# Optimization experiments

Measured on AMD Instinct MI355X. Metric: run time of the kernel, lower is better.

The kernel has to match this reference:

```python
import jax, jax.numpy as jnp
import numpy as np

N_BLOCK = 3; EMBED = 256; N_HEAD = 8; HEAD = EMBED // N_HEAD
N_AGENT = 8; SEQ = 256; BATCH = 64; ACT_DIM = 32
DECAY_SCALE = 1.0
EPS = 1e-6


def _decay_matrix():
    # Per-head decay kappas as in Mava Sable, decay over timesteps (pos // n_agent), causal mask.
    gammas = (1.0 - jnp.exp(jnp.linspace(jnp.log(1.0 / 32.0), jnp.log(1.0 / 512.0), N_HEAD))) * DECAY_SCALE
    t = (jnp.arange(SEQ) // N_AGENT).astype(jnp.float32)
    diff = t[:, None] - t[None, :]
    causal = jnp.arange(SEQ)[:, None] >= jnp.arange(SEQ)[None, :]
    return jnp.where(causal[None], gammas[:, None, None] ** diff[None], 0.0)  # [H,S,S]


def rmsnorm(x, scale):
    return x * jax.lax.rsqrt(jnp.mean(x * x, -1, keepdims=True) + EPS) * scale


def groupnorm(x, scale, bias):
    # GroupNorm with n_head groups over the feature dim, per position.
    B, S, E = x.shape
    xg = x.reshape(B, S, N_HEAD, HEAD)
    mu = xg.mean(-1, keepdims=True)
    var = ((xg - mu) ** 2).mean(-1, keepdims=True)
    xn = ((xg - mu) * jax.lax.rsqrt(var + 1e-5)).reshape(B, S, E)
    return xn * scale + bias


def retention(q_in, k_in, v_in, wq, wk, wv, wg, wo, gns, gnb, decay):
    # Parallel multi-scale retention: (Q K^T * D) V, groupnorm, swish gate from query input.
    B, S, E = q_in.shape
    q = (q_in @ wq).reshape(B, S, N_HEAD, HEAD).transpose(0, 2, 1, 3)
    k = (k_in @ wk).reshape(B, S, N_HEAD, HEAD).transpose(0, 2, 1, 3) / jnp.sqrt(jnp.float32(HEAD))
    v = (v_in @ wv).reshape(B, S, N_HEAD, HEAD).transpose(0, 2, 1, 3)
    scores = jnp.einsum('bhnd,bhmd->bhnm', q, k) * decay[None]
    ret = jnp.einsum('bhnm,bhmd->bhnd', scores, v)
    ret = groupnorm(ret.transpose(0, 2, 1, 3).reshape(B, S, E), gns, gnb)
    return (jax.nn.swish(q_in @ wg) * ret) @ wo


def swiglu(x, wg, w1, w2):
    return (jax.nn.swish(x @ wg) * (x @ w1)) @ w2


def forward(action, obs_rep, w_enc, ln0, wq1, wk1, wv1, wg1, wo1, gns1, gnb1, ln1,
            wq2, wk2, wv2, wg2, wo2, gns2, gnb2, ln2, swg, sw1, sw2, ln3,
            hw1, hb1, hln, hw2, hb2):
    decay = _decay_matrix()
    x = rmsnorm(jax.nn.gelu(action @ w_enc), ln0)
    for b in range(N_BLOCK):
        r1 = retention(x, x, x, wq1[b], wk1[b], wv1[b], wg1[b], wo1[b], gns1[b], gnb1[b], decay)
        x = rmsnorm(x + r1, ln1[b])
        r2 = retention(obs_rep, x, x, wq2[b], wk2[b], wv2[b], wg2[b], wo2[b], gns2[b], gnb2[b], decay)
        x = rmsnorm(obs_rep + r2, ln2[b])
        x = rmsnorm(x + swiglu(x, swg[b], sw1[b], sw2[b]), ln3[b])
    h = rmsnorm(jax.nn.gelu(x @ hw1 + hb1), hln)
    return h @ hw2 + hb2


def setup_inputs() -> dict:
    key = jax.random.key(0)
    ks = jax.random.split(key, 24)
    E, A, NB = EMBED, ACT_DIM, N_BLOCK
    s = 0.02
    return {
        'action': jax.random.uniform(ks[0], (BATCH, SEQ, A), jnp.float32),
        'obs_rep': jax.random.normal(ks[1], (BATCH, SEQ, E), jnp.float32),
        'w_enc': jax.random.normal(ks[2], (A, E), jnp.float32) * s,
        'ln0': jnp.ones((E,), jnp.float32),
        'wq1': jax.random.normal(ks[3], (NB, E, E), jnp.float32) * s,
        'wk1': jax.random.normal(ks[4], (NB, E, E), jnp.float32) * s,
        'wv1': jax.random.normal(ks[5], (NB, E, E), jnp.float32) * s,
        'wg1': jax.random.normal(ks[6], (NB, E, E), jnp.float32) * s,
        'wo1': jax.random.normal(ks[7], (NB, E, E), jnp.float32) * s,
        'gns1': jnp.ones((NB, E), jnp.float32),
        'gnb1': jnp.zeros((NB, E), jnp.float32),
        'ln1': jnp.ones((NB, E), jnp.float32),
        'wq2': jax.random.normal(ks[8], (NB, E, E), jnp.float32) * s,
        'wk2': jax.random.normal(ks[9], (NB, E, E), jnp.float32) * s,
        'wv2': jax.random.normal(ks[10], (NB, E, E), jnp.float32) * s,
        'wg2': jax.random.normal(ks[11], (NB, E, E), jnp.float32) * s,
        'wo2': jax.random.normal(ks[12], (NB, E, E), jnp.float32) * s,
        'gns2': jnp.ones((NB, E), jnp.float32),
        'gnb2': jnp.zeros((NB, E), jnp.float32),
        'ln2': jnp.ones((NB, E), jnp.float32),
        'swg': jax.random.normal(ks[13], (NB, E, E), jnp.float32) * s,
        'sw1': jax.random.normal(ks[14], (NB, E, E), jnp.float32) * s,
        'sw2': jax.random.normal(ks[15], (NB, E, E), jnp.float32) * s,
        'ln3': jnp.ones((NB, E), jnp.float32),
        'hw1': jax.random.normal(ks[16], (E, E), jnp.float32) * s,
        'hb1': jnp.zeros((E,), jnp.float32),
        'hln': jnp.ones((E,), jnp.float32),
        'hw2': jax.random.normal(ks[17], (E, A), jnp.float32) * s,
        'hb2': jnp.zeros((A,), jnp.float32),
    }


def reference(action, obs_rep, w_enc, ln0, wq1, wk1, wv1, wg1, wo1, gns1, gnb1, ln1,
              wq2, wk2, wv2, wg2, wo2, gns2, gnb2, ln2, swg, sw1, sw2, ln3,
              hw1, hb1, hln, hw2, hb2):
    return forward(action, obs_rep, w_enc, ln0, wq1, wk1, wv1, wg1, wo1, gns1, gnb1, ln1,
                   wq2, wk2, wv2, wg2, wo2, gns2, gnb2, ln2, swg, sw1, sw2, ln3,
                   hw1, hb1, hln, hw2, hb2)
```

## Files before the change

kernel.cpp:

```cpp
#include <hip/hip_runtime.h>
#include <cstdint>
#include <cmath>

typedef __attribute__((ext_vector_type(8))) short short8;
typedef __attribute__((ext_vector_type(4))) float floatx4;

#define DEV static __device__ __forceinline__

DEV float bf2f(uint16_t u) {
    union { uint32_t i; float f; } v; v.i = ((uint32_t)u) << 16; return v.f;
}
DEV uint16_t f2bf(float f) {
    union { float f; uint32_t i; } v; v.f = f;
    uint32_t r = (v.i + 0x7FFFu + ((v.i >> 16) & 1u)) >> 16;
    return (uint16_t)r;
}
DEV float swishf(float x) { return x / (1.f + __expf(-x)); }
DEV float geluf(float x) {
    const float c = 0.7978845608028654f;
    float t = tanhf(c * (x + 0.044715f * x * x * x));
    return 0.5f * x * (1.f + t);
}

#define CHUNK_E 8192
#define MAT_E   65536
#define APAD    264


struct TArg { const float* src[15]; };

__global__ __launch_bounds__(256) void tpose_k(TArg ta, uint16_t* __restrict__ arena) {
    int z = blockIdx.z;
    const float* src; uint16_t* dst;
    if (z == 0) {
        if (blockIdx.y) return;
        src = ta.src[0]; dst = arena;
    } else if (z <= 39) {
        int q = z - 1; int ti = q / 3, s = q % 3;
        src = ta.src[1 + ti] + (size_t)s * 65536;
        dst = arena + CHUNK_E + (size_t)(ti * 3 + s) * MAT_E;
    } else {
        src = ta.src[14]; dst = arena + CHUNK_E + (size_t)39 * MAT_E;
    }
    int k0 = blockIdx.y << 5;
    int n0 = blockIdx.x << 6;
    __shared__ __align__(16) uint16_t tile[32][72];
    int t = threadIdx.x;
    {
        int r = t >> 3, c = (t & 7) << 3;
        const float* s0 = src + (size_t)(k0 + r) * 256 + n0 + c;
        float4 f0 = *(const float4*)s0;
        float4 f1 = *(const float4*)(s0 + 4);
        tile[r][c + 0] = f2bf(f0.x); tile[r][c + 1] = f2bf(f0.y);
        tile[r][c + 2] = f2bf(f0.z); tile[r][c + 3] = f2bf(f0.w);
        tile[r][c + 4] = f2bf(f1.x); tile[r][c + 5] = f2bf(f1.y);
        tile[r][c + 6] = f2bf(f1.z); tile[r][c + 7] = f2bf(f1.w);
    }
    __syncthreads();
    {
        int n = t >> 2, c = (t & 3) << 3;
        uint16_t tmp[8];
#pragma unroll
        for (int j = 0; j < 8; ++j) tmp[j] = tile[c + j][n];
        *(uint4*)&dst[(size_t)(k0 >> 5) * CHUNK_E + (size_t)(n0 + n) * 32 + c] = *(uint4*)tmp;
    }
}

struct SegArgs {
    const float* action; const float* obs;
    uint16_t *actb, *obsb, *xb, *bq, *bk, *bv, *bg, *brg;
    const float *ln0, *hb1, *hln, *hw2, *hb2;
    float* outp;
    float l2g[8];
};

enum { EP_NONE = 0, EP_GELU_RMS = 1, EP_RESID_RMS = 2 };
enum { EP2_NONE = 0, EP2_SWIGLU = 1 };

template<int EPI, int K, int LDA, bool OG, int LDO, bool RL>
DEV void gemm_u(int m0,
                const uint16_t* __restrict__ A,
                const uint16_t* __restrict__ Wt,
                uint16_t* __restrict__ Og,
                uint16_t* __restrict__ Ol,
                const float* __restrict__ bias,
                const uint16_t* __restrict__ Rg,
                const uint16_t* __restrict__ Rl,
                const float* __restrict__ lnw,
                float (&rowsum)[8][32])
{
    const int t = threadIdx.x;
    const int w = t >> 6, lane = t & 63, l16 = lane & 15, lg = lane >> 4;
    constexpr int NC = K / 32;

    floatx4 acc[2][2];
#pragma unroll
    for (int i = 0; i < 2; ++i)
#pragma unroll
        for (int j = 0; j < 2; ++j) acc[i][j] = (floatx4){0.f, 0.f, 0.f, 0.f};

#pragma unroll
    for (int kc = 0; kc < NC; ++kc) {
        short8 aF[2], bF[2];
#pragma unroll
        for (int rt = 0; rt < 2; ++rt) {
            int row = (rt << 4) + l16;
            if constexpr (LDA != 0)
                aF[rt] = *(const short8*)(A + (size_t)row * LDA + (kc << 5) + (lg << 3));
            else
                aF[rt] = *(const short8*)(A + (size_t)(m0 + row) * K + (kc << 5) + (lg << 3));
        }
#pragma unroll
        for (int ct = 0; ct < 2; ++ct)
            bF[ct] = *(const short8*)(Wt + (size_t)kc * CHUNK_E +
                                      (size_t)((w << 5) + (ct << 4) + l16) * 32 + (lg << 3));
#pragma unroll
        for (int rt = 0; rt < 2; ++rt)
#pragma unroll
            for (int ct = 0; ct < 2; ++ct)
                acc[rt][ct] = __builtin_amdgcn_mfma_f32_16x16x32_bf16(
                    aF[rt], bF[ct], acc[rt][ct], 0, 0, 0);
    }

    float v[2][2][4];
#pragma unroll
    for (int rt = 0; rt < 2; ++rt)
#pragma unroll
        for (int ct = 0; ct < 2; ++ct)
#pragma unroll
            for (int r = 0; r < 4; ++r) {
                int row = (rt << 4) + (lg << 2) + r;
                int col = (w << 5) + (ct << 4) + l16;
                float x = acc[rt][ct][r];
                if constexpr (EPI == EP_GELU_RMS) {
                    if (bias) x += bias[col];
                    x = geluf(x);
                }
                if constexpr (EPI == EP_RESID_RMS) {
                    if constexpr (RL) x += bf2f(Rl[(size_t)row * APAD + col]);
                    else              x += bf2f(Rg[(size_t)(m0 + row) * 256 + col]);
                }
                v[rt][ct][r] = x;
            }

    if constexpr (EPI == EP_GELU_RMS || EPI == EP_RESID_RMS) {
#pragma unroll
        for (int rt = 0; rt < 2; ++rt)
#pragma unroll
            for (int r = 0; r < 4; ++r) {
                float p = v[rt][0][r] * v[rt][0][r] + v[rt][1][r] * v[rt][1][r];
                p += __shfl_xor(p, 1, 64); p += __shfl_xor(p, 2, 64);
                p += __shfl_xor(p, 4, 64); p += __shfl_xor(p, 8, 64);
                int row = (rt << 4) + (lg << 2) + r;
                if (l16 == 0) rowsum[w][row] = p;
            }
        __syncthreads();
#pragma unroll
        for (int rt = 0; rt < 2; ++rt)
#pragma unroll
            for (int r = 0; r < 4; ++r) {
                int row = (rt << 4) + (lg << 2) + r;
                float tot = rowsum[0][row] + rowsum[1][row] + rowsum[2][row] + rowsum[3][row]
                          + rowsum[4][row] + rowsum[5][row] + rowsum[6][row] + rowsum[7][row];
                float rn = rsqrtf(tot * (1.f / 256.f) + 1e-6f);
#pragma unroll
                for (int ct = 0; ct < 2; ++ct) {
                    int col = (w << 5) + (ct << 4) + l16;
                    uint16_t bb = f2bf(v[rt][ct][r] * rn * lnw[col]);
                    if constexpr (OG)
                        Og[(size_t)(m0 + row) * 256 + col] = bb;
                    if constexpr (LDO != 0)
                        Ol[(size_t)row * LDO + col] = bb;
                }
            }
        __syncthreads();
    } else {
#pragma unroll
        for (int rt = 0; rt < 2; ++rt)
#pragma unroll
            for (int ct = 0; ct < 2; ++ct)
#pragma unroll
                for (int r = 0; r < 4; ++r) {
                    int row = (rt << 4) + (lg << 2) + r;
                    int col = (w << 5) + (ct << 4) + l16;
                    uint16_t bb = f2bf(v[rt][ct][r]);
                    if constexpr (OG)
                        Og[(size_t)(m0 + row) * 256 + col] = bb;
                    if constexpr (LDO != 0)
                        Ol[(size_t)row * LDO + col] = bb;
                }
    }
}

template<int EPI, int LDA>
DEV void gemm2_u(int m0, const uint16_t* __restrict__ A,
                 const uint16_t* __restrict__ W1, const uint16_t* __restrict__ W2,
                 uint16_t* __restrict__ O1, uint16_t* __restrict__ O2,
                 uint16_t* __restrict__ Ol)
{
    const int t = threadIdx.x;
    const int w = t >> 6, lane = t & 63, l16 = lane & 15, lg = lane >> 4;

    floatx4 a1[2][2], a2[2][2];
#pragma unroll
    for (int i = 0; i < 2; ++i)
#pragma unroll
        for (int j = 0; j < 2; ++j) {
            a1[i][j] = (floatx4){0.f, 0.f, 0.f, 0.f};
            a2[i][j] = (floatx4){0.f, 0.f, 0.f, 0.f};
        }

#pragma unroll
    for (int kc = 0; kc < 8; ++kc) {
        short8 aF[2], b1[2], b2[2];
#pragma unroll
        for (int rt = 0; rt < 2; ++rt) {
            int row = (rt << 4) + l16;
            if constexpr (LDA != 0)
                aF[rt] = *(const short8*)(A + (size_t)row * LDA + (kc << 5) + (lg << 3));
            else
                aF[rt] = *(const short8*)(A + (size_t)(m0 + row) * 256 + (kc << 5) + (lg << 3));
        }
        size_t woff = (size_t)kc * CHUNK_E + (size_t)((w << 5) + l16) * 32 + (lg << 3);
#pragma unroll
        for (int ct = 0; ct < 2; ++ct) {
            b1[ct] = *(const short8*)(W1 + woff + (size_t)(ct << 4) * 32);
            b2[ct] = *(const short8*)(W2 + woff + (size_t)(ct << 4) * 32);
        }
#pragma unroll
        for (int rt = 0; rt < 2; ++rt)
#pragma unroll
            for (int ct = 0; ct < 2; ++ct) {
                a1[rt][ct] = __builtin_amdgcn_mfma_f32_16x16x32_bf16(aF[rt], b1[ct], a1[rt][ct], 0, 0, 0);
                a2[rt][ct] = __builtin_amdgcn_mfma_f32_16x16x32_bf16(aF[rt], b2[ct], a2[rt][ct], 0, 0, 0);
            }
    }

#pragma unroll
    for (int rt = 0; rt < 2; ++rt)
#pragma unroll
        for (int ct = 0; ct < 2; ++ct)
#pragma unroll
            for (int r = 0; r < 4; ++r) {
                int row = (rt << 4) + (lg << 2) + r;
                int col = (w << 5) + (ct << 4) + l16;
                if constexpr (EPI == EP2_NONE) {
                    size_t idx = (size_t)(m0 + row) * 256 + col;
                    O1[idx] = f2bf(a1[rt][ct][r]);
                    O2[idx] = f2bf(a2[rt][ct][r]);
                } else {
                    Ol[(size_t)row * APAD + col] = f2bf(swishf(a1[rt][ct][r]) * a2[rt][ct][r]);
                }
            }
}

template<int LDA>
DEV void gemm4_u(int m0, const uint16_t* __restrict__ A,
                 const uint16_t* __restrict__ W0, const uint16_t* __restrict__ W1,
                 const uint16_t* __restrict__ W2, const uint16_t* __restrict__ W3,
                 uint16_t* __restrict__ O0, uint16_t* __restrict__ O1,
                 uint16_t* __restrict__ O2, uint16_t* __restrict__ O3)
{
    const int t = threadIdx.x;
    const int w = t >> 6, lane = t & 63, l16 = lane & 15, lg = lane >> 4;
    const uint16_t* Wm[4] = {W0, W1, W2, W3};
    uint16_t* Om[4] = {O0, O1, O2, O3};

    floatx4 acc[4][2][2];
#pragma unroll
    for (int m = 0; m < 4; ++m)
#pragma unroll
        for (int i = 0; i < 2; ++i)
#pragma unroll
            for (int j = 0; j < 2; ++j) acc[m][i][j] = (floatx4){0.f, 0.f, 0.f, 0.f};

#pragma unroll
    for (int kc = 0; kc < 8; ++kc) {
        short8 aF[2];
#pragma unroll
        for (int rt = 0; rt < 2; ++rt) {
            int row = (rt << 4) + l16;
            if constexpr (LDA != 0)
                aF[rt] = *(const short8*)(A + (size_t)row * LDA + (kc << 5) + (lg << 3));
            else
                aF[rt] = *(const short8*)(A + (size_t)(m0 + row) * 256 + (kc << 5) + (lg << 3));
        }
        size_t woff = (size_t)kc * CHUNK_E + (size_t)((w << 5) + l16) * 32 + (lg << 3);
        short8 bF[4][2];
#pragma unroll
        for (int m = 0; m < 4; ++m)
#pragma unroll
            for (int ct = 0; ct < 2; ++ct)
                bF[m][ct] = *(const short8*)(Wm[m] + woff + (size_t)(ct << 4) * 32);
#pragma unroll
        for (int m = 0; m < 4; ++m)
#pragma unroll
            for (int rt = 0; rt < 2; ++rt)
#pragma unroll
                for (int ct = 0; ct < 2; ++ct)
                    acc[m][rt][ct] = __builtin_amdgcn_mfma_f32_16x16x32_bf16(
                        aF[rt], bF[m][ct], acc[m][rt][ct], 0, 0, 0);
    }

#pragma unroll
    for (int m = 0; m < 4; ++m)
#pragma unroll
        for (int rt = 0; rt < 2; ++rt)
#pragma unroll
            for (int ct = 0; ct < 2; ++ct)
#pragma unroll
                for (int r = 0; r < 4; ++r) {
                    int row = (rt << 4) + (lg << 2) + r;
                    int col = (w << 5) + (ct << 4) + l16;
                    Om[m][(size_t)(m0 + row) * 256 + col] = f2bf(acc[m][rt][ct][r]);
                }
}

template<int LDA1>
DEV void gemm22_u(int m0, const uint16_t* __restrict__ A1, const uint16_t* __restrict__ A2,
                  const uint16_t* __restrict__ W0, const uint16_t* __restrict__ W1,
                  const uint16_t* __restrict__ W2, const uint16_t* __restrict__ W3,
                  uint16_t* __restrict__ O0, uint16_t* __restrict__ O1,
                  uint16_t* __restrict__ O2, uint16_t* __restrict__ O3)
{
    const int t = threadIdx.x;
    const int w = t >> 6, lane = t & 63, l16 = lane & 15, lg = lane >> 4;
    const uint16_t* Wm[4] = {W0, W1, W2, W3};
    uint16_t* Om[4] = {O0, O1, O2, O3};

    floatx4 acc[4][2][2];
#pragma unroll
    for (int m = 0; m < 4; ++m)
#pragma unroll
        for (int i = 0; i < 2; ++i)
#pragma unroll
            for (int j = 0; j < 2; ++j) acc[m][i][j] = (floatx4){0.f, 0.f, 0.f, 0.f};

#pragma unroll
    for (int kc = 0; kc < 8; ++kc) {
        short8 a1F[2], a2F[2];
#pragma unroll
        for (int rt = 0; rt < 2; ++rt) {
            int row = (rt << 4) + l16;
            a1F[rt] = *(const short8*)(A1 + (size_t)row * LDA1 + (kc << 5) + (lg << 3));
            a2F[rt] = *(const short8*)(A2 + (size_t)(m0 + row) * 256 + (kc << 5) + (lg << 3));
        }
        size_t woff = (size_t)kc * CHUNK_E + (size_t)((w << 5) + l16) * 32 + (lg << 3);
        short8 bF[4][2];
#pragma unroll
        for (int m = 0; m < 4; ++m)
#pragma unroll
            for (int ct = 0; ct < 2; ++ct)
                bF[m][ct] = *(const short8*)(Wm[m] + woff + (size_t)(ct << 4) * 32);
#pragma unroll
        for (int m = 0; m < 4; ++m)
#pragma unroll
            for (int rt = 0; rt < 2; ++rt)
#pragma unroll
                for (int ct = 0; ct < 2; ++ct)
                    acc[m][rt][ct] = __builtin_amdgcn_mfma_f32_16x16x32_bf16(
                        (m < 2) ? a1F[rt] : a2F[rt], bF[m][ct], acc[m][rt][ct], 0, 0, 0);
    }

#pragma unroll
    for (int m = 0; m < 4; ++m)
#pragma unroll
        for (int rt = 0; rt < 2; ++rt)
#pragma unroll
            for (int ct = 0; ct < 2; ++ct)
#pragma unroll
                for (int r = 0; r < 4; ++r) {
                    int row = (rt << 4) + (lg << 2) + r;
                    int col = (w << 5) + (ct << 4) + l16;
                    Om[m][(size_t)(m0 + row) * 256 + col] = f2bf(acc[m][rt][ct][r]);
                }
}

DEV int rowbase(int blk) { return (blk & 63) * 256 + (blk >> 6) * 32; }


__global__ __launch_bounds__(512, 4) void seg0_k(SegArgs sa, const uint16_t* __restrict__ wenc,
                                                 const uint16_t* __restrict__ wq,
                                                 const uint16_t* __restrict__ wk,
                                                 const uint16_t* __restrict__ wv,
                                                 const uint16_t* __restrict__ wg)
{
    __shared__ float rowsum[8][32];
    __shared__ __align__(16) uint16_t actS[32][40];
    __shared__ __align__(16) uint16_t T0[32][APAD];
    const int t = threadIdx.x;
    const int m0 = rowbase(blockIdx.x);
    if (t < 256) {
        int r = t >> 3, c = (t & 7) << 2;
        float4 f = *(const float4*)(sa.action + (size_t)(m0 + r) * 32 + c);
        uint16_t tmp[4] = { f2bf(f.x), f2bf(f.y), f2bf(f.z), f2bf(f.w) };
        *(uint2*)&actS[r][c] = *(uint2*)tmp;
    }
    {
        const float4* ob = (const float4*)sa.obs + (size_t)m0 * 64;
        uint2* od = (uint2*)sa.obsb + (size_t)m0 * 64;
#pragma unroll
        for (int j = 0; j < 4; ++j) {
            float4 f = ob[(j << 9) + t];
            uint16_t tmp[4] = { f2bf(f.x), f2bf(f.y), f2bf(f.z), f2bf(f.w) };
            od[(j << 9) + t] = *(uint2*)tmp;
        }
    }
    __syncthreads();
    gemm_u<EP_GELU_RMS, 32, 40, true, APAD, false>(m0, &actS[0][0], wenc,
        sa.xb, &T0[0][0], nullptr, nullptr, nullptr, sa.ln0, rowsum);
    gemm4_u<APAD>(m0, &T0[0][0], wq, wk, wv, wg, sa.bq, sa.bk, sa.bv, sa.bg);
}

__global__ __launch_bounds__(512, 4) void attn_k(SegArgs sa, const float* __restrict__ gns,
                                                 const float* __restrict__ gnb)
{
    __shared__ __align__(16) uint16_t QS[256][40];
    __shared__ __align__(16) uint16_t Ks[256][40];
    __shared__ __align__(16) uint16_t Vt[32][264];
    const int b = blockIdx.x & 63, h = blockIdx.x >> 6;
    const float l2g = sa.l2g[h];
    const int t = threadIdx.x, w = t >> 6, lane = t & 63, l16 = lane & 15, lg = lane >> 4;
    const size_t base = ((size_t)b * 256) * 256 + (size_t)h * 32;
    const uint16_t *q = sa.bq, *kbuf = sa.bk, *vbuf = sa.bv, *g = sa.bg;
    uint16_t* out = sa.brg;

    if (t < 256) {
        const uint4* qr = (const uint4*)(q + base + (size_t)t * 256);
        *(uint4*)&QS[t][0] = qr[0]; *(uint4*)&QS[t][8] = qr[1];
        *(uint4*)&QS[t][16] = qr[2]; *(uint4*)&QS[t][24] = qr[3];
        const uint4* kr = (const uint4*)(kbuf + base + (size_t)t * 256);
        *(uint4*)&Ks[t][0] = kr[0]; *(uint4*)&Ks[t][8] = kr[1];
        *(uint4*)&Ks[t][16] = kr[2]; *(uint4*)&Ks[t][24] = kr[3];
    } else {
        int c = t - 256;
        union { uint4 v4[4]; uint16_t u[32]; } vv;
        const uint4* vr = (const uint4*)(vbuf + base + (size_t)c * 256);
        vv.v4[0] = vr[0]; vv.v4[1] = vr[1]; vv.v4[2] = vr[2]; vv.v4[3] = vr[3];
#pragma unroll
        for (int d = 0; d < 32; ++d) Vt[d][c] = vv.u[d];
    }
    __syncthreads();

    const int iA = w, iB = 15 - w;
    short8 qFA = *(const short8*)&QS[(iA << 4) + l16][lg << 3];
    short8 qFB = *(const short8*)&QS[(iB << 4) + l16][lg << 3];

    const float invsq = 0.17677669529663687f;

    floatx4 raccA[2], raccB[2];
    raccA[0] = (floatx4){0,0,0,0}; raccA[1] = (floatx4){0,0,0,0};
    raccB[0] = (floatx4){0,0,0,0}; raccB[1] = (floatx4){0,0,0,0};

    auto do_strip = [&](int si, short8 qF, floatx4 (&racc)[2]) {
        const int jtmax = ((si << 4) + 15) >> 5;
        for (int jt = 0; jt <= jtmax; ++jt) {
            const int j0 = jt << 5;
            floatx4 sacc[2];
            sacc[0] = (floatx4){0,0,0,0}; sacc[1] = (floatx4){0,0,0,0};
            short8 kF[2];
#pragma unroll
            for (int ct = 0; ct < 2; ++ct)
                kF[ct] = *(const short8*)&Ks[j0 + (ct << 4) + l16][lg << 3];
#pragma unroll
            for (int ct = 0; ct < 2; ++ct)
                sacc[ct] = __builtin_amdgcn_mfma_f32_16x16x32_bf16(
                    qF, kF[ct], sacc[ct], 0, 0, 0);
#pragma unroll
            for (int ct = 0; ct < 2; ++ct)
#pragma unroll
                for (int r = 0; r < 4; ++r) {
                    int row16 = (lg << 2) + r;
                    int i = (si << 4) + row16;
                    int j = j0 + (ct << 4) + l16;
                    float svv = 0.f;
                    if (i >= j)
                        svv = sacc[ct][r] * invsq *
                              exp2f((float)((i >> 3) - (j >> 3)) * l2g);
                    QS[(si << 4) + row16][(ct << 4) + l16] = f2bf(svv);
                }
            short8 vF[2];
#pragma unroll
            for (int ct = 0; ct < 2; ++ct)
                vF[ct] = *(const short8*)&Vt[(ct << 4) + l16][j0 + (lg << 3)];
            short8 sF = *(const short8*)&QS[(si << 4) + l16][lg << 3];
#pragma unroll
            for (int ct = 0; ct < 2; ++ct)
                racc[ct] = __builtin_amdgcn_mfma_f32_16x16x32_bf16(
                    sF, vF[ct], racc[ct], 0, 0, 0);
        }
    };
    do_strip(iA, qFA, raccA);
    do_strip(iB, qFB, raccB);

    auto epi = [&](int si, floatx4 (&racc)[2]) {
#pragma unroll
        for (int r = 0; r < 4; ++r) {
            float v0 = racc[0][r], v1 = racc[1][r];
            float s1 = v0 + v1, s2 = v0 * v0 + v1 * v1;
            s1 += __shfl_xor(s1, 1, 64); s2 += __shfl_xor(s2, 1, 64);
            s1 += __shfl_xor(s1, 2, 64); s2 += __shfl_xor(s2, 2, 64);
            s1 += __shfl_xor(s1, 4, 64); s2 += __shfl_xor(s2, 4, 64);
            s1 += __shfl_xor(s1, 8, 64); s2 += __shfl_xor(s2, 8, 64);
            float mu = s1 * (1.f / 32.f);
            float var = s2 * (1.f / 32.f) - mu * mu;
            float rstd = rsqrtf(var + 1e-5f);
            int srow = (si << 4) + (lg << 2) + r;
            size_t obase = ((size_t)b * 256 + srow) * 256 + (size_t)h * 32;
#pragma unroll
            for (int ct = 0; ct < 2; ++ct) {
                int d = (ct << 4) + l16;
                float x = ct ? v1 : v0;
                float y = (x - mu) * rstd * gns[h * 32 + d] + gnb[h * 32 + d];
                float gv = swishf(bf2f(g[obase + d]));
                out[obase + d] = f2bf(y * gv);
            }
        }
    };
    epi(iA, raccA);
    epi(iB, raccB);
}

__global__ __launch_bounds__(512, 4) void g1_k(SegArgs sa,
    const uint16_t* __restrict__ wo, const float* __restrict__ ln1,
    const uint16_t* __restrict__ wq, const uint16_t* __restrict__ wk,
    const uint16_t* __restrict__ wv, const uint16_t* __restrict__ wg)
{
    __shared__ float rowsum[8][32];
    __shared__ __align__(16) uint16_t T0[32][APAD];
    const int m0 = rowbase(blockIdx.x);
    gemm_u<EP_RESID_RMS, 256, 0, false, APAD, false>(m0, sa.brg, wo,
        nullptr, &T0[0][0], nullptr, sa.xb, nullptr, ln1, rowsum);
    gemm22_u<APAD>(m0, &T0[0][0], sa.obsb, wk, wv, wq, wg,
                   sa.bk, sa.bv, sa.bq, sa.bg);
}

__global__ __launch_bounds__(512, 4) void g2_k(SegArgs sa,
    const uint16_t* __restrict__ wo, const float* __restrict__ ln2,
    const uint16_t* __restrict__ wswg, const uint16_t* __restrict__ wsw1,
    const uint16_t* __restrict__ wsw2, const float* __restrict__ ln3,
    const uint16_t* __restrict__ nwq, const uint16_t* __restrict__ nwk,
    const uint16_t* __restrict__ nwv, const uint16_t* __restrict__ nwg)
{
    __shared__ float rowsum[8][32];
    __shared__ __align__(16) uint16_t T0[32][APAD];
    __shared__ __align__(16) uint16_t T1[32][APAD];
    const int m0 = rowbase(blockIdx.x);
    gemm_u<EP_RESID_RMS, 256, 0, false, APAD, false>(m0, sa.brg, wo,
        nullptr, &T0[0][0], nullptr, sa.obsb, nullptr, ln2, rowsum);
    gemm2_u<EP2_SWIGLU, APAD>(m0, &T0[0][0], wswg, wsw1, nullptr, nullptr, &T1[0][0]);
    __syncthreads();
    gemm_u<EP_RESID_RMS, 256, APAD, true, APAD, true>(m0, &T1[0][0], wsw2,
        sa.xb, &T0[0][0], nullptr, nullptr, &T0[0][0], ln3, rowsum);
    if (nwq) {
        gemm4_u<APAD>(m0, &T0[0][0], nwq, nwk, nwv, nwg, sa.bq, sa.bk, sa.bv, sa.bg);
    }
}

__global__ __launch_bounds__(512, 4) void head_k(SegArgs sa, const uint16_t* __restrict__ hw1t)
{
    __shared__ float rowsum[8][32];
    __shared__ float w2s[8192];
    __shared__ __align__(16) uint16_t T0[32][APAD];
    const int t = threadIdx.x;
    const int m0 = rowbase(blockIdx.x);
#pragma unroll
    for (int j = 0; j < 16; ++j) w2s[(j << 9) + t] = sa.hw2[(j << 9) + t];
    gemm_u<EP_GELU_RMS, 256, 0, false, APAD, false>(m0, sa.xb, hw1t,
        nullptr, &T0[0][0], sa.hb1, nullptr, nullptr, sa.hln, rowsum);
    {
        int n = t & 31, rs = t >> 5;
#pragma unroll
        for (int rr = 0; rr < 2; ++rr) {
            int lrow = (rr << 4) + rs;
            float a0 = sa.hb2[n];
#pragma unroll 8
            for (int kk = 0; kk < 256; ++kk)
                a0 += bf2f(T0[lrow][kk]) * w2s[kk * 32 + n];
            sa.outp[(size_t)(m0 + lrow) * 32 + n] = a0;
        }
    }
}

extern "C" void kernel_launch(void* const* d_in, const int* in_sizes, int n_in,
                              void* d_out, int out_size, void* d_ws, size_t ws_size,
                              hipStream_t stream)
{
    const float* action = (const float*)d_in[0];
    const float* obs    = (const float*)d_in[1];
    const float* w_enc  = (const float*)d_in[2];
    const float* ln0    = (const float*)d_in[3];
    const float* wq1 = (const float*)d_in[4];
    const float* wk1 = (const float*)d_in[5];
    const float* wv1 = (const float*)d_in[6];
    const float* wg1 = (const float*)d_in[7];
    const float* wo1 = (const float*)d_in[8];
    const float* gns1 = (const float*)d_in[9];
    const float* gnb1 = (const float*)d_in[10];
    const float* ln1  = (const float*)d_in[11];
    const float* wq2 = (const float*)d_in[12];
    const float* wk2 = (const float*)d_in[13];
    const float* wv2 = (const float*)d_in[14];
    const float* wg2 = (const float*)d_in[15];
    const float* wo2 = (const float*)d_in[16];
    const float* gns2 = (const float*)d_in[17];
    const float* gnb2 = (const float*)d_in[18];
    const float* ln2  = (const float*)d_in[19];
    const float* swgp = (const float*)d_in[20];
    const float* sw1p = (const float*)d_in[21];
    const float* sw2p = (const float*)d_in[22];
    const float* ln3  = (const float*)d_in[23];
    const float* hw1  = (const float*)d_in[24];
    const float* hb1  = (const float*)d_in[25];
    const float* hln  = (const float*)d_in[26];
    const float* hw2  = (const float*)d_in[27];
    const float* hb2  = (const float*)d_in[28];

    char* ws = (char*)d_ws;
    uint16_t* wt   = (uint16_t*)(ws + 0);
    uint16_t* actb = (uint16_t*)(ws + 6291456);
    uint16_t* obsb = (uint16_t*)(ws + 7340032);
    uint16_t* xb   = (uint16_t*)(ws + 15728640);
    uint16_t* bq   = (uint16_t*)(ws + 24117248);
    uint16_t* bk   = (uint16_t*)(ws + 32505856);
    uint16_t* bv   = (uint16_t*)(ws + 40894464);
    uint16_t* bg   = (uint16_t*)(ws + 49283072);
    uint16_t* brg  = (uint16_t*)(ws + 57671680);

    uint16_t* wtenc = wt;
    uint16_t* hw1t  = wt + CHUNK_E + (size_t)39 * MAT_E;
    auto WTp = [&](int ti, int s) { return wt + CHUNK_E + (size_t)(ti * 3 + s) * MAT_E; };

    TArg ta;
    ta.src[0] = w_enc;
    ta.src[1] = wq1;  ta.src[2] = wk1;  ta.src[3] = wv1;  ta.src[4] = wg1;  ta.src[5] = wo1;
    ta.src[6] = wq2;  ta.src[7] = wk2;  ta.src[8] = wv2;  ta.src[9] = wg2;  ta.src[10] = wo2;
    ta.src[11] = swgp; ta.src[12] = sw1p; ta.src[13] = sw2p; ta.src[14] = hw1;
    tpose_k<<<dim3(4, 8, 41), 256, 0, stream>>>(ta, wt);

    SegArgs sa;
    sa.action = action; sa.obs = obs;
    sa.actb = actb; sa.obsb = obsb; sa.xb = xb;
    sa.bq = bq; sa.bk = bk; sa.bv = bv; sa.bg = bg; sa.brg = brg;
    sa.ln0 = ln0; sa.hb1 = hb1; sa.hln = hln; sa.hw2 = hw2; sa.hb2 = hb2;
    sa.outp = (float*)d_out;
    {
        const double a = log(1.0 / 32.0), bb = log(1.0 / 512.0);
        for (int hh = 0; hh < 8; ++hh) {
            double lg = a + (bb - a) * hh / 7.0;
            double gam = 1.0 - exp(lg);
            sa.l2g[hh] = (float)(log(gam) / log(2.0));
        }
    }

    dim3 GB(512), TB(512);
    seg0_k<<<GB, TB, 0, stream>>>(sa, wtenc, WTp(0, 0), WTp(1, 0), WTp(2, 0), WTp(3, 0));
    for (int b3 = 0; b3 < 3; ++b3) {
        attn_k<<<GB, TB, 0, stream>>>(sa, gns1 + b3 * 256, gnb1 + b3 * 256);
        g1_k<<<GB, TB, 0, stream>>>(sa, WTp(4, b3), ln1 + b3 * 256,
                                    WTp(5, b3), WTp(6, b3), WTp(7, b3), WTp(8, b3));
        attn_k<<<GB, TB, 0, stream>>>(sa, gns2 + b3 * 256, gnb2 + b3 * 256);
        g2_k<<<GB, TB, 0, stream>>>(sa, WTp(9, b3), ln2 + b3 * 256,
                                    WTp(10, b3), WTp(11, b3), WTp(12, b3), ln3 + b3 * 256,
                                    b3 < 2 ? WTp(0, b3 + 1) : nullptr,
                                    b3 < 2 ? WTp(1, b3 + 1) : nullptr,
                                    b3 < 2 ? WTp(2, b3 + 1) : nullptr,
                                    b3 < 2 ? WTp(3, b3 + 1) : nullptr);
    }
    head_k<<<GB, TB, 0, stream>>>(sa, hw1t);
}
```

Measured before the change: 566.3 us.

## Restructure fused GEMMs with split-K and weight-split warp tiling plus LDS staging

Replaces the 32-column-per-warp GEMM helpers with 64-column warp tiles. Single-output GEMMs now use split-K across two warp groups with an LDS reduction buffer, and paired GEMMs assign each weight matrix to half of the warps. Residual and obs inputs are staged into shared memory before use, and the head kernel reuses the reduction buffer to hold hw2. The intent is to cut redundant A-fragment loads and register pressure per warp, at the cost of extra LDS traffic and barriers for the reductions.

```diff
diff --git a/kernel.cpp b/kernel.cpp
--- a/kernel.cpp
+++ b/kernel.cpp
@@ -74,306 +74,271 @@
     float l2g[8];
 };
 
-enum { EP_NONE = 0, EP_GELU_RMS = 1, EP_RESID_RMS = 2 };
 enum { EP2_NONE = 0, EP2_SWIGLU = 1 };
 
-template<int EPI, int K, int LDA, bool OG, int LDO, bool RL>
-DEV void gemm_u(int m0,
-                const uint16_t* __restrict__ A,
-                const uint16_t* __restrict__ Wt,
-                uint16_t* __restrict__ Og,
-                uint16_t* __restrict__ Ol,
-                const float* __restrict__ bias,
-                const uint16_t* __restrict__ Rg,
-                const uint16_t* __restrict__ Rl,
-                const float* __restrict__ lnw,
-                float (&rowsum)[8][32])
+DEV void stage32(const uint16_t* __restrict__ g, int m0, uint16_t* __restrict__ lds) {
+    const int t = threadIdx.x;
+#pragma unroll
+    for (int j = 0; j < 2; ++j) {
+        int u = t + (j << 9);
+        int r = u >> 5, cc = (u & 31) << 3;
+        *(short8*)(lds + (size_t)r * APAD + cc) =
+            *(const short8*)(g + (size_t)(m0 + r) * 256 + cc);
+    }
+}
+
+template<bool AL, bool OG, bool RL, bool GELU>
+DEV void gemm_ks(int m0, const uint16_t* __restrict__ A, const uint16_t* __restrict__ Wt,
+                 uint16_t* __restrict__ Og, uint16_t* __restrict__ Ol,
+                 const float* __restrict__ bias,
+                 const uint16_t* __restrict__ Rg, const uint16_t* __restrict__ Rl,
+                 const float* __restrict__ lnw,
+                 float (&rowsum)[8][32], float (&red)[4][32][64])
 {
     const int t = threadIdx.x;
     const int w = t >> 6, lane = t & 63, l16 = lane & 15, lg = lane >> 4;
-    constexpr int NC = K / 32;
-
-    floatx4 acc[2][2];
+    const int wc = w & 3, cb = wc << 6;
+    const int kbase = (w >> 2) << 2;
+
+    floatx4 acc[2][4];
 #pragma unroll
     for (int i = 0; i < 2; ++i)
 #pragma unroll
-        for (int j = 0; j < 2; ++j) acc[i][j] = (floatx4){0.f, 0.f, 0.f, 0.f};
-
-#pragma unroll
-    for (int kc = 0; kc < NC; ++kc) {
-        short8 aF[2], bF[2];
+        for (int j = 0; j < 4; ++j) acc[i][j] = (floatx4){0.f, 0.f, 0.f, 0.f};
+
+#pragma unroll
+    for (int k2 = 0; k2 < 4; ++k2) {
+        const int kc = kbase + k2;
+        short8 aF[2], bF[4];
 #pragma unroll
         for (int rt = 0; rt < 2; ++rt) {
             int row = (rt << 4) + l16;
-            if constexpr (LDA != 0)
-                aF[rt] = *(const short8*)(A + (size_t)row * LDA + (kc << 5) + (lg << 3));
+            if constexpr (AL)
+                aF[rt] = *(const short8*)(A + (size_t)row * APAD + (kc << 5) + (lg << 3));
             else
-                aF[rt] = *(const short8*)(A + (size_t)(m0 + row) * K + (kc << 5) + (lg << 3));
-        }
-#pragma unroll
-        for (int ct = 0; ct < 2; ++ct)
+                aF[rt] = *(const short8*)(A + (size_t)(m0 + row) * 256 + (kc << 5) + (lg << 3));
+        }
+#pragma unroll
+        for (int ct = 0; ct < 4; ++ct)
             bF[ct] = *(const short8*)(Wt + (size_t)kc * CHUNK_E +
-                                      (size_t)((w << 5) + (ct << 4) + l16) * 32 + (lg << 3));
+                                      (size_t)(cb + (ct << 4) + l16) * 32 + (lg << 3));
 #pragma unroll
         for (int rt = 0; rt < 2; ++rt)
 #pragma unroll
-            for (int ct = 0; ct < 2; ++ct)
+            for (int ct = 0; ct < 4; ++ct)
                 acc[rt][ct] = __builtin_amdgcn_mfma_f32_16x16x32_bf16(
                     aF[rt], bF[ct], acc[rt][ct], 0, 0, 0);
     }
 
-    float v[2][2][4];
-#pragma unroll
-    for (int rt = 0; rt < 2; ++rt)
-#pragma unroll
-        for (int ct = 0; ct < 2; ++ct)
+    if (w >= 4) {
+#pragma unroll
+        for (int rt = 0; rt < 2; ++rt)
+#pragma unroll
+            for (int ct = 0; ct < 4; ++ct)
+#pragma unroll
+                for (int r = 0; r < 4; ++r)
+                    red[wc][(rt << 4) | (ct << 2) | r][lane] = acc[rt][ct][r];
+    }
+    __syncthreads();
+
+    float v[2][4][4];
+    if (w < 4) {
+#pragma unroll
+        for (int rt = 0; rt < 2; ++rt)
+#pragma unroll
+            for (int ct = 0; ct < 4; ++ct)
+#pragma unroll
+                for (int r = 0; r < 4; ++r) {
+                    int row = (rt << 4) + (lg << 2) + r;
+                    int col = cb + (ct << 4) + l16;
+                    float x = acc[rt][ct][r] + red[wc][(rt << 4) | (ct << 2) | r][lane];
+                    if constexpr (GELU) {
+                        if (bias) x += bias[col];
+                        x = geluf(x);
+                    } else {
+                        if constexpr (RL) x += bf2f(Rl[(size_t)row * APAD + col]);
+                        else              x += bf2f(Rg[(size_t)(m0 + row) * 256 + col]);
+                    }
+                    v[rt][ct][r] = x;
+                }
+#pragma unroll
+        for (int rt = 0; rt < 2; ++rt)
 #pragma unroll
             for (int r = 0; r < 4; ++r) {
-                int row = (rt << 4) + (lg << 2) + r;
-                int col = (w << 5) + (ct << 4) + l16;
-                float x = acc[rt][ct][r];
-                if constexpr (EPI == EP_GELU_RMS) {
-                    if (bias) x += bias[col];
-                    x = geluf(x);
-                }
-                if constexpr (EPI == EP_RESID_RMS) {
-                    if constexpr (RL) x += bf2f(Rl[(size_t)row * APAD + col]);
-                    else              x += bf2f(Rg[(size_t)(m0 + row) * 256 + col]);
-                }
-                v[rt][ct][r] = x;
-            }
-
-    if constexpr (EPI == EP_GELU_RMS || EPI == EP_RESID_RMS) {
-#pragma unroll
-        for (int rt = 0; rt < 2; ++rt)
-#pragma unroll
-            for (int r = 0; r < 4; ++r) {
-                float p = v[rt][0][r] * v[rt][0][r] + v[rt][1][r] * v[rt][1][r];
+                float p = 0.f;
+#pragma unroll
+                for (int ct = 0; ct < 4; ++ct) p += v[rt][ct][r] * v[rt][ct][r];
                 p += __shfl_xor(p, 1, 64); p += __shfl_xor(p, 2, 64);
                 p += __shfl_xor(p, 4, 64); p += __shfl_xor(p, 8, 64);
                 int row = (rt << 4) + (lg << 2) + r;
                 if (l16 == 0) rowsum[w][row] = p;
             }
-        __syncthreads();
+    }
+    __syncthreads();
+    if (w < 4) {
 #pragma unroll
         for (int rt = 0; rt < 2; ++rt)
 #pragma unroll
             for (int r = 0; r < 4; ++r) {
                 int row = (rt << 4) + (lg << 2) + r;
-                float tot = rowsum[0][row] + rowsum[1][row] + rowsum[2][row] + rowsum[3][row]
-                          + rowsum[4][row] + rowsum[5][row] + rowsum[6][row] + rowsum[7][row];
+                float tot = rowsum[0][row] + rowsum[1][row] + rowsum[2][row] + rowsum[3][row];
                 float rn = rsqrtf(tot * (1.f / 256.f) + 1e-6f);
 #pragma unroll
-                for (int ct = 0; ct < 2; ++ct) {
-                    int col = (w << 5) + (ct << 4) + l16;
+                for (int ct = 0; ct < 4; ++ct) {
+                    int col = cb + (ct << 4) + l16;
                     uint16_t bb = f2bf(v[rt][ct][r] * rn * lnw[col]);
                     if constexpr (OG)
                         Og[(size_t)(m0 + row) * 256 + col] = bb;
-                    if constexpr (LDO != 0)
-                        Ol[(size_t)row * LDO + col] = bb;
+                    Ol[(size_t)row * APAD + col] = bb;
                 }
             }
-        __syncthreads();
-    } else {
+    }
+    __syncthreads();
+}
+
+template<int EPI, bool AL>
+DEV void gemm2_ws(int m0, const uint16_t* __restrict__ A,
+                  const uint16_t* __restrict__ W1, const uint16_t* __restrict__ W2,
+                  uint16_t* __restrict__ O1, uint16_t* __restrict__ O2,
+                  uint16_t* __restrict__ Ol, float (&red)[4][32][64])
+{
+    const int t = threadIdx.x;
+    const int w = t >> 6, lane = t & 63, l16 = lane & 15, lg = lane >> 4;
+    const int wc = w & 3, cb = wc << 6;
+    const uint16_t* W = (w < 4) ? W1 : W2;
+
+    floatx4 acc[2][4];
+#pragma unroll
+    for (int i = 0; i < 2; ++i)
+#pragma unroll
+        for (int j = 0; j < 4; ++j) acc[i][j] = (floatx4){0.f, 0.f, 0.f, 0.f};
+
+#pragma unroll
+    for (int kc = 0; kc < 8; ++kc) {
+        short8 aF[2], bF[4];
+#pragma unroll
+        for (int rt = 0; rt < 2; ++rt) {
+            int row = (rt << 4) + l16;
+            if constexpr (AL)
+                aF[rt] = *(const short8*)(A + (size_t)row * APAD + (kc << 5) + (lg << 3));
+            else
+                aF[rt] = *(const short8*)(A + (size_t)(m0 + row) * 256 + (kc << 5) + (lg << 3));
+        }
+#pragma unroll
+        for (int ct = 0; ct < 4; ++ct)
+            bF[ct] = *(const short8*)(W + (size_t)kc * CHUNK_E +
+                                      (size_t)(cb + (ct << 4) + l16) * 32 + (lg << 3));
 #pragma unroll
         for (int rt = 0; rt < 2; ++rt)
 #pragma unroll
-            for (int ct = 0; ct < 2; ++ct)
+            for (int ct = 0; ct < 4; ++ct)
+                acc[rt][ct] = __builtin_amdgcn_mfma_f32_16x16x32_bf16(
+                    aF[rt], bF[ct], acc[rt][ct], 0, 0, 0);
+    }
+
+    if constexpr (EPI == EP2_NONE) {
+        uint16_t* O = (w < 4) ? O1 : O2;
+#pragma unroll
+        for (int rt = 0; rt < 2; ++rt)
+#pragma unroll
+            for (int ct = 0; ct < 4; ++ct)
 #pragma unroll
                 for (int r = 0; r < 4; ++r) {
                     int row = (rt << 4) + (lg << 2) + r;
-                    int col = (w << 5) + (ct << 4) + l16;
-                    uint16_t bb = f2bf(v[rt][ct][r]);
-                    if constexpr (OG)
-                        Og[(size_t)(m0 + row) * 256 + col] = bb;
-                    if constexpr (LDO != 0)
-                        Ol[(size_t)row * LDO + col] = bb;
+                    int col = cb + (ct << 4) + l16;
+                    O[(size_t)(m0 + row) * 256 + col] = f2bf(acc[rt][ct][r]);
                 }
-    }
-}
-
-template<int EPI, int LDA>
-DEV void gemm2_u(int m0, const uint16_t* __restrict__ A,
-                 const uint16_t* __restrict__ W1, const uint16_t* __restrict__ W2,
-                 uint16_t* __restrict__ O1, uint16_t* __restrict__ O2,
-                 uint16_t* __restrict__ Ol)
+    } else {
+        if (w >= 4) {
+#pragma unroll
+            for (int rt = 0; rt < 2; ++rt)
+#pragma unroll
+                for (int ct = 0; ct < 4; ++ct)
+#pragma unroll
+                    for (int r = 0; r < 4; ++r)
+                        red[wc][(rt << 4) | (ct << 2) | r][lane] = acc[rt][ct][r];
+        }
+        __syncthreads();
+        if (w < 4) {
+#pragma unroll
+            for (int rt = 0; rt < 2; ++rt)
+#pragma unroll
+                for (int ct = 0; ct < 4; ++ct)
+#pragma unroll
+                    for (int r = 0; r < 4; ++r) {
+                        int row = (rt << 4) + (lg << 2) + r;
+                        int col = cb + (ct << 4) + l16;
+                        float up = red[wc][(rt << 4) | (ct << 2) | r][lane];
+                        Ol[(size_t)row * APAD + col] = f2bf(swishf(acc[rt][ct][r]) * up);
+                    }
+        }
+    }
+}
+
+DEV void gemm_enc(int m0, const uint16_t* __restrict__ A, const uint16_t* __restrict__ Wt,
+                  uint16_t* __restrict__ Og, uint16_t* __restrict__ Ol,
+                  const float* __restrict__ lnw, float (&rowsum)[8][32])
 {
     const int t = threadIdx.x;
     const int w = t >> 6, lane = t & 63, l16 = lane & 15, lg = lane >> 4;
 
-    floatx4 a1[2][2], a2[2][2];
+    floatx4 acc[2][2];
 #pragma unroll
     for (int i = 0; i < 2; ++i)
 #pragma unroll
-        for (int j = 0; j < 2; ++j) {
-            a1[i][j] = (floatx4){0.f, 0.f, 0.f, 0.f};
-            a2[i][j] = (floatx4){0.f, 0.f, 0.f, 0.f};
-        }
-
-#pragma unroll
-    for (int kc = 0; kc < 8; ++kc) {
-        short8 aF[2], b1[2], b2[2];
-#pragma unroll
-        for (int rt = 0; rt < 2; ++rt) {
-            int row = (rt << 4) + l16;
-            if constexpr (LDA != 0)
-                aF[rt] = *(const short8*)(A + (size_t)row * LDA + (kc << 5) + (lg << 3));
-            else
-                aF[rt] = *(const short8*)(A + (size_t)(m0 + row) * 256 + (kc << 5) + (lg << 3));
-        }
-        size_t woff = (size_t)kc * CHUNK_E + (size_t)((w << 5) + l16) * 32 + (lg << 3);
-#pragma unroll
-        for (int ct = 0; ct < 2; ++ct) {
-            b1[ct] = *(const short8*)(W1 + woff + (size_t)(ct << 4) * 32);
-            b2[ct] = *(const short8*)(W2 + woff + (size_t)(ct << 4) * 32);
-        }
-#pragma unroll
-        for (int rt = 0; rt < 2; ++rt)
+        for (int j = 0; j < 2; ++j) acc[i][j] = (floatx4){0.f, 0.f, 0.f, 0.f};
+
+    short8 aF[2], bF[2];
+#pragma unroll
+    for (int rt = 0; rt < 2; ++rt)
+        aF[rt] = *(const short8*)(A + (size_t)((rt << 4) + l16) * 40 + (lg << 3));
+#pragma unroll
+    for (int ct = 0; ct < 2; ++ct)
+        bF[ct] = *(const short8*)(Wt + (size_t)((w << 5) + (ct << 4) + l16) * 32 + (lg << 3));
+#pragma unroll
+    for (int rt = 0; rt < 2; ++rt)
+#pragma unroll
+        for (int ct = 0; ct < 2; ++ct)
+            acc[rt][ct] = __builtin_amdgcn_mfma_f32_16x16x32_bf16(
+                aF[rt], bF[ct], acc[rt][ct], 0, 0, 0);
+
+    float v[2][2][4];
+#pragma unroll
+    for (int rt = 0; rt < 2; ++rt)
+#pragma unroll
+        for (int ct = 0; ct < 2; ++ct)
+#pragma unroll
+            for (int r = 0; r < 4; ++r)
+                v[rt][ct][r] = geluf(acc[rt][ct][r]);
+
+#pragma unroll
+    for (int rt = 0; rt < 2; ++rt)
+#pragma unroll
+        for (int r = 0; r < 4; ++r) {
+            float p = v[rt][0][r] * v[rt][0][r] + v[rt][1][r] * v[rt][1][r];
+            p += __shfl_xor(p, 1, 64); p += __shfl_xor(p, 2, 64);
+            p += __shfl_xor(p, 4, 64); p += __shfl_xor(p, 8, 64);
+            int row = (rt << 4) + (lg << 2) + r;
+            if (l16 == 0) rowsum[w][row] = p;
+        }
+    __syncthreads();
+#pragma unroll
+    for (int rt = 0; rt < 2; ++rt)
+#pragma unroll
+        for (int r = 0; r < 4; ++r) {
+            int row = (rt << 4) + (lg << 2) + r;
+            float tot = rowsum[0][row] + rowsum[1][row] + rowsum[2][row] + rowsum[3][row]
+                      + rowsum[4][row] + rowsum[5][row] + rowsum[6][row] + rowsum[7][row];
+            float rn = rsqrtf(tot * (1.f / 256.f) + 1e-6f);
 #pragma unroll
             for (int ct = 0; ct < 2; ++ct) {
-                a1[rt][ct] = __builtin_amdgcn_mfma_f32_16x16x32_bf16(aF[rt], b1[ct], a1[rt][ct], 0, 0, 0);
-                a2[rt][ct] = __builtin_amdgcn_mfma_f32_16x16x32_bf16(aF[rt], b2[ct], a2[rt][ct], 0, 0, 0);
+                int col = (w << 5) + (ct << 4) + l16;
+                uint16_t bb = f2bf(v[rt][ct][r] * rn * lnw[col]);
+                Og[(size_t)(m0 + row) * 256 + col] = bb;
+                Ol[(size_t)row * APAD + col] = bb;
             }
-    }
-
-#pragma unroll
-    for (int rt = 0; rt < 2; ++rt)
-#pragma unroll
-        for (int ct = 0; ct < 2; ++ct)
-#pragma unroll
-            for (int r = 0; r < 4; ++r) {
-                int row = (rt << 4) + (lg << 2) + r;
-                int col = (w << 5) + (ct << 4) + l16;
-                if constexpr (EPI == EP2_NONE) {
-                    size_t idx = (size_t)(m0 + row) * 256 + col;
-                    O1[idx] = f2bf(a1[rt][ct][r]);
-                    O2[idx] = f2bf(a2[rt][ct][r]);
-                } else {
-                    Ol[(size_t)row * APAD + col] = f2bf(swishf(a1[rt][ct][r]) * a2[rt][ct][r]);
-                }
-            }
-}
-
-template<int LDA>
-DEV void gemm4_u(int m0, const uint16_t* __restrict__ A,
-                 const uint16_t* __restrict__ W0, const uint16_t* __restrict__ W1,
-                 const uint16_t* __restrict__ W2, const uint16_t* __restrict__ W3,
-                 uint16_t* __restrict__ O0, uint16_t* __restrict__ O1,
-                 uint16_t* __restrict__ O2, uint16_t* __restrict__ O3)
-{
-    const int t = threadIdx.x;
-    const int w = t >> 6, lane = t & 63, l16 = lane & 15, lg = lane >> 4;
-    const uint16_t* Wm[4] = {W0, W1, W2, W3};
-    uint16_t* Om[4] = {O0, O1, O2, O3};
-
-    floatx4 acc[4][2][2];
-#pragma unroll
-    for (int m = 0; m < 4; ++m)
-#pragma unroll
-        for (int i = 0; i < 2; ++i)
-#pragma unroll
-            for (int j = 0; j < 2; ++j) acc[m][i][j] = (floatx4){0.f, 0.f, 0.f, 0.f};
-
-#pragma unroll
-    for (int kc = 0; kc < 8; ++kc) {
-        short8 aF[2];
-#pragma unroll
-        for (int rt = 0; rt < 2; ++rt) {
-            int row = (rt << 4) + l16;
-            if constexpr (LDA != 0)
-                aF[rt] = *(const short8*)(A + (size_t)row * LDA + (kc << 5) + (lg << 3));
-            else
-                aF[rt] = *(const short8*)(A + (size_t)(m0 + row) * 256 + (kc << 5) + (lg << 3));
-        }
-        size_t woff = (size_t)kc * CHUNK_E + (size_t)((w << 5) + l16) * 32 + (lg << 3);
-        short8 bF[4][2];
-#pragma unroll
-        for (int m = 0; m < 4; ++m)
-#pragma unroll
-            for (int ct = 0; ct < 2; ++ct)
-                bF[m][ct] = *(const short8*)(Wm[m] + woff + (size_t)(ct << 4) * 32);
-#pragma unroll
-        for (int m = 0; m < 4; ++m)
-#pragma unroll
-            for (int rt = 0; rt < 2; ++rt)
-#pragma unroll
-                for (int ct = 0; ct < 2; ++ct)
-                    acc[m][rt][ct] = __builtin_amdgcn_mfma_f32_16x16x32_bf16(
-                        aF[rt], bF[m][ct], acc[m][rt][ct], 0, 0, 0);
-    }
-
-#pragma unroll
-    for (int m = 0; m < 4; ++m)
-#pragma unroll
-        for (int rt = 0; rt < 2; ++rt)
-#pragma unroll
-            for (int ct = 0; ct < 2; ++ct)
-#pragma unroll
-                for (int r = 0; r < 4; ++r) {
-                    int row = (rt << 4) + (lg << 2) + r;
-                    int col = (w << 5) + (ct << 4) + l16;
-                    Om[m][(size_t)(m0 + row) * 256 + col] = f2bf(acc[m][rt][ct][r]);
-                }
-}
-
-template<int LDA1>
-DEV void gemm22_u(int m0, const uint16_t* __restrict__ A1, const uint16_t* __restrict__ A2,
-                  const uint16_t* __restrict__ W0, const uint16_t* __restrict__ W1,
-                  const uint16_t* __restrict__ W2, const uint16_t* __restrict__ W3,
-                  uint16_t* __restrict__ O0, uint16_t* __restrict__ O1,
-                  uint16_t* __restrict__ O2, uint16_t* __restrict__ O3)
-{
-    const int t = threadIdx.x;
-    const int w = t >> 6, lane = t & 63, l16 = lane & 15, lg = lane >> 4;
-    const uint16_t* Wm[4] = {W0, W1, W2, W3};
-    uint16_t* Om[4] = {O0, O1, O2, O3};
-
-    floatx4 acc[4][2][2];
-#pragma unroll
-    for (int m = 0; m < 4; ++m)
-#pragma unroll
-        for (int i = 0; i < 2; ++i)
-#pragma unroll
-            for (int j = 0; j < 2; ++j) acc[m][i][j] = (floatx4){0.f, 0.f, 0.f, 0.f};
-
-#pragma unroll
-    for (int kc = 0; kc < 8; ++kc) {
-        short8 a1F[2], a2F[2];
-#pragma unroll
-        for (int rt = 0; rt < 2; ++rt) {
-            int row = (rt << 4) + l16;
-            a1F[rt] = *(const short8*)(A1 + (size_t)row * LDA1 + (kc << 5) + (lg << 3));
-            a2F[rt] = *(const short8*)(A2 + (size_t)(m0 + row) * 256 + (kc << 5) + (lg << 3));
-        }
-        size_t woff = (size_t)kc * CHUNK_E + (size_t)((w << 5) + l16) * 32 + (lg << 3);
-        short8 bF[4][2];
-#pragma unroll
-        for (int m = 0; m < 4; ++m)
-#pragma unroll
-            for (int ct = 0; ct < 2; ++ct)
-                bF[m][ct] = *(const short8*)(Wm[m] + woff + (size_t)(ct << 4) * 32);
-#pragma unroll
-        for (int m = 0; m < 4; ++m)
-#pragma unroll
-            for (int rt = 0; rt < 2; ++rt)
-#pragma unroll
-                for (int ct = 0; ct < 2; ++ct)
-                    acc[m][rt][ct] = __builtin_amdgcn_mfma_f32_16x16x32_bf16(
-                        (m < 2) ? a1F[rt] : a2F[rt], bF[m][ct], acc[m][rt][ct], 0, 0, 0);
-    }
-
-#pragma unroll
-    for (int m = 0; m < 4; ++m)
-#pragma unroll
-        for (int rt = 0; rt < 2; ++rt)
-#pragma unroll
-            for (int ct = 0; ct < 2; ++ct)
-#pragma unroll
-                for (int r = 0; r < 4; ++r) {
-                    int row = (rt << 4) + (lg << 2) + r;
-                    int col = (w << 5) + (ct << 4) + l16;
-                    Om[m][(size_t)(m0 + row) * 256 + col] = f2bf(acc[m][rt][ct][r]);
-                }
+        }
+    __syncthreads();
 }
 
 DEV int rowbase(int blk) { return (blk & 63) * 256 + (blk >> 6) * 32; }
@@ -386,6 +351,7 @@
                                                  const uint16_t* __restrict__ wg)
 {
     __shared__ float rowsum[8][32];
+    __shared__ float red[4][32][64];
     __shared__ __align__(16) uint16_t actS[32][40];
     __shared__ __align__(16) uint16_t T0[32][APAD];
     const int t = threadIdx.x;
@@ -407,9 +373,9 @@
         }
     }
     __syncthreads();
-    gemm_u<EP_GELU_RMS, 32, 40, true, APAD, false>(m0, &actS[0][0], wenc,
-        sa.xb, &T0[0][0], nullptr, nullptr, nullptr, sa.ln0, rowsum);
-    gemm4_u<APAD>(m0, &T0[0][0], wq, wk, wv, wg, sa.bq, sa.bk, sa.bv, sa.bg);
+    gemm_enc(m0, &actS[0][0], wenc, sa.xb, &T0[0][0], sa.ln0, rowsum);
+    gemm2_ws<EP2_NONE, true>(m0, &T0[0][0], wq, wk, sa.bq, sa.bk, nullptr, red);
+    gemm2_ws<EP2_NONE, true>(m0, &T0[0][0], wv, wg, sa.bv, sa.bg, nullptr, red);
 }
 
 __global__ __launch_bounds__(512, 4) void attn_k(SegArgs sa, const float* __restrict__ gns,
@@ -527,12 +493,18 @@
     const uint16_t* __restrict__ wv, const uint16_t* __restrict__ wg)
 {
     __shared__ float rowsum[8][32];
+    __shared__ float red[4][32][64];
     __shared__ __align__(16) uint16_t T0[32][APAD];
+    __shared__ __align__(16) uint16_t T1[32][APAD];
     const int m0 = rowbase(blockIdx.x);
-    gemm_u<EP_RESID_RMS, 256, 0, false, APAD, false>(m0, sa.brg, wo,
-        nullptr, &T0[0][0], nullptr, sa.xb, nullptr, ln1, rowsum);
-    gemm22_u<APAD>(m0, &T0[0][0], sa.obsb, wk, wv, wq, wg,
-                   sa.bk, sa.bv, sa.bq, sa.bg);
+    stage32(sa.brg, m0, &T1[0][0]);
+    __syncthreads();
+    gemm_ks<true, false, false, false>(m0, &T1[0][0], wo,
+        nullptr, &T0[0][0], nullptr, sa.xb, nullptr, ln1, rowsum, red);
+    stage32(sa.obsb, m0, &T1[0][0]);
+    gemm2_ws<EP2_NONE, true>(m0, &T0[0][0], wk, wv, sa.bk, sa.bv, nullptr, red);
+    __syncthreads();
+    gemm2_ws<EP2_NONE, true>(m0, &T1[0][0], wq, wg, sa.bq, sa.bg, nullptr, red);
 }
 
 __global__ __launch_bounds__(512, 4) void g2_k(SegArgs sa,
@@ -543,31 +515,37 @@
     const uint16_t* __restrict__ nwv, const uint16_t* __restrict__ nwg)
 {
     __shared__ float rowsum[8][32];
+    __shared__ float red[4][32][64];
     __shared__ __align__(16) uint16_t T0[32][APAD];
     __shared__ __align__(16) uint16_t T1[32][APAD];
     const int m0 = rowbase(blockIdx.x);
-    gemm_u<EP_RESID_RMS, 256, 0, false, APAD, false>(m0, sa.brg, wo,
-        nullptr, &T0[0][0], nullptr, sa.obsb, nullptr, ln2, rowsum);
-    gemm2_u<EP2_SWIGLU, APAD>(m0, &T0[0][0], wswg, wsw1, nullptr, nullptr, &T1[0][0]);
-    __syncthreads();
-    gemm_u<EP_RESID_RMS, 256, APAD, true, APAD, true>(m0, &T1[0][0], wsw2,
-        sa.xb, &T0[0][0], nullptr, nullptr, &T0[0][0], ln3, rowsum);
+    stage32(sa.brg, m0, &T1[0][0]);
+    __syncthreads();
+    gemm_ks<true, false, false, false>(m0, &T1[0][0], wo,
+        nullptr, &T0[0][0], nullptr, sa.obsb, nullptr, ln2, rowsum, red);
+    gemm2_ws<EP2_SWIGLU, true>(m0, &T0[0][0], wswg, wsw1, nullptr, nullptr, &T1[0][0], red);
+    __syncthreads();
+    gemm_ks<true, true, true, false>(m0, &T1[0][0], wsw2,
+        sa.xb, &T0[0][0], nullptr, nullptr, &T0[0][0], ln3, rowsum, red);
     if (nwq) {
-        gemm4_u<APAD>(m0, &T0[0][0], nwq, nwk, nwv, nwg, sa.bq, sa.bk, sa.bv, sa.bg);
+        gemm2_ws<EP2_NONE, true>(m0, &T0[0][0], nwq, nwk, sa.bq, sa.bk, nullptr, red);
+        gemm2_ws<EP2_NONE, true>(m0, &T0[0][0], nwv, nwg, sa.bv, sa.bg, nullptr, red);
     }
 }
 
 __global__ __launch_bounds__(512, 4) void head_k(SegArgs sa, const uint16_t* __restrict__ hw1t)
 {
     __shared__ float rowsum[8][32];
-    __shared__ float w2s[8192];
+    __shared__ float red[4][32][64];
     __shared__ __align__(16) uint16_t T0[32][APAD];
     const int t = threadIdx.x;
     const int m0 = rowbase(blockIdx.x);
+    gemm_ks<false, false, false, true>(m0, sa.xb, hw1t,
+        nullptr, &T0[0][0], sa.hb1, nullptr, nullptr, sa.hln, rowsum, red);
+    float* w2s = &red[0][0][0];
 #pragma unroll
     for (int j = 0; j < 16; ++j) w2s[(j << 9) + t] = sa.hw2[(j << 9) + t];
-    gemm_u<EP_GELU_RMS, 256, 0, false, APAD, false>(m0, sa.xb, hw1t,
-        nullptr, &T0[0][0], sa.hb1, nullptr, nullptr, sa.hln, rowsum);
+    __syncthreads();
     {
         int n = t & 31, rs = t >> 5;
 #pragma unroll
```

Measured after the change: 496.1 us. -12.4%, faster.
